# Optimization experiments

Hardware: AMD Instinct MI355X
Metric: run time of the kernel (lower is better)

The kernel has to match this reference:

```python
import jax, jax.numpy as jnp
import numpy as np

N = 8192      # total nodes = B * NPG
D = 512       # in_dim = hidden_dim = out_dim
E = 131072    # edges
B = 16        # graphs (selected_idx batch)
NPG = 512     # nodes per graph
S = 128       # selected nodes per graph
L = 3         # conv layers
EPS = 1e-5


def setup_inputs() -> dict:
    key = jax.random.key(0)
    ks = jax.random.split(key, 16)
    scale = 0.02
    return {
        "x": jax.random.normal(ks[0], (N, D), dtype=jnp.float32),
        "edge_index": jax.random.randint(ks[1], (2, E), 0, N),
        "selected_idx": jax.random.randint(ks[2], (B, S), 0, NPG),
        "edge_label": jax.random.randint(ks[3], (E,), 0, 4),
        # per-layer EdgeConv MLP params (stacked over L layers)
        "conv_W1": jax.random.normal(ks[4], (L, 2 * D, D), dtype=jnp.float32) * scale,
        "conv_b1": jnp.full((L, D), 0.01, dtype=jnp.float32),
        "conv_W2": jax.random.normal(ks[5], (L, D, D), dtype=jnp.float32) * scale,
        "conv_b2": jnp.full((L, D), 0.01, dtype=jnp.float32),
        # shared layer norms
        "ln1_g": jnp.ones((D,), dtype=jnp.float32),
        "ln1_b": jnp.zeros((D,), dtype=jnp.float32),
        "ln2_g": jnp.ones((D,), dtype=jnp.float32),
        "ln2_b": jnp.zeros((D,), dtype=jnp.float32),
        # final FFN
        "ffn_W1": jax.random.normal(ks[6], (D, D), dtype=jnp.float32) * scale,
        "ffn_b1": jnp.full((D,), 0.01, dtype=jnp.float32),
        "ffn_W2": jax.random.normal(ks[7], (D, D), dtype=jnp.float32) * scale,
        "ffn_b2": jnp.full((D,), 0.01, dtype=jnp.float32),
    }


def _layer_norm(x, g, b):
    mu = jnp.mean(x, axis=-1, keepdims=True)
    var = jnp.mean(jnp.square(x - mu), axis=-1, keepdims=True)
    return (x - mu) * jax.lax.rsqrt(var + EPS) * g + b


def reference(x, edge_index, selected_idx, edge_label,
              conv_W1, conv_b1, conv_W2, conv_b2,
              ln1_g, ln1_b, ln2_g, ln2_b,
              ffn_W1, ffn_b1, ffn_W2, ffn_b2):
    src = edge_index[0]  # x_j source nodes
    dst = edge_index[1]  # x_i target nodes (aggregation index)
    for l in range(L):
        residual = x
        h = _layer_norm(x, ln1_g, ln1_b)
        hi = h[dst]                                   # [E, D]
        hj = h[src]                                   # [E, D]
        ef = jnp.concatenate([hi, hj - hi], axis=1)   # [E, 2D]
        m = jnp.maximum(ef @ conv_W1[l] + conv_b1[l], 0.0) @ conv_W2[l] + conv_b2[l]
        agg = jax.ops.segment_max(m, dst, num_segments=N)  # max-aggregate [N, D]
        agg = jnp.where(jnp.isfinite(agg), agg, 0.0)       # nodes w/o in-edges -> 0
        x = jnp.maximum(agg, 0.0) + residual
    residual = x
    h = _layer_norm(x, ln2_g, ln2_b)
    y = jnp.maximum(h @ ffn_W1 + ffn_b1, 0.0) @ ffn_W2 + ffn_b2
    x = y + residual
    x = x.reshape(B, NPG, D)
    idx = jnp.broadcast_to(selected_idx[:, :, None], (B, S, D))
    return jnp.take_along_axis(x, idx, axis=1)  # [B, S, D]
```

## Files before the change

kernel.cpp:

```cpp
#include <hip/hip_runtime.h>
#include <stdint.h>

#define NN 8192
#define DD 512
#define EE 131072
#define BBATCH 16
#define NPG 512
#define SSEL 128
#define LL 3

typedef unsigned short u16;
typedef __bf16 bf16x8 __attribute__((ext_vector_type(8)));
typedef float f32x4 __attribute__((ext_vector_type(4)));
typedef float f32x2 __attribute__((ext_vector_type(2)));
typedef u16 u16x8 __attribute__((ext_vector_type(8)));

__device__ __forceinline__ float bf2f(u16 u) {
    union { unsigned i; float f; } v; v.i = ((unsigned)u) << 16; return v.f;
}
__device__ __forceinline__ u16 f2bf(float f) {
    union { unsigned i; float f; } v; v.f = f;
    unsigned i = v.i;
    return (u16)((i + 0x7FFFu + ((i >> 16) & 1u)) >> 16);
}

__device__ __forceinline__ unsigned pk_bf16(float s0, float s1) {
#if __has_builtin(__builtin_amdgcn_cvt_pk_bf16_f32)
    typedef __bf16 bf16x2 __attribute__((ext_vector_type(2)));
    union { bf16x2 v; unsigned u; } r;
    r.v = __builtin_amdgcn_cvt_pk_bf16_f32(s0, s1);
    return r.u;
#else
    unsigned r0 = __float_as_uint(s0);
    r0 = (r0 + 0x7FFFu + ((r0 >> 16) & 1u)) >> 16;
    unsigned r1 = __float_as_uint(s1);
    r1 = (r1 + 0x7FFFu + ((r1 >> 16) & 1u)) & 0xffff0000u;
    return r0 | r1;
#endif
}

__device__ __forceinline__ void async_cp16(const u16* g, u16* l) {
    __builtin_amdgcn_global_load_lds(
        (const __attribute__((address_space(1))) unsigned int*)g,
        (__attribute__((address_space(3))) unsigned int*)l, 16, 0, 0);
}

__global__ __launch_bounds__(256) void ln_fused(const float* __restrict__ xin,
                                                float* __restrict__ agg_io,
                                                float* __restrict__ xout,
                                                const float* __restrict__ g,
                                                const float* __restrict__ b,
                                                u16* __restrict__ h, int doAdd) {
    int row = blockIdx.x * 4 + (threadIdx.x >> 6);
    int lane = threadIdx.x & 63;
    const f32x4* x4 = (const f32x4*)(xin + (size_t)row * DD);
    f32x4 p = x4[lane * 2], q = x4[lane * 2 + 1];
    if (doAdd) {
        const f32x4* a4 = (const f32x4*)(agg_io + (size_t)row * DD);
        f32x4 pa = a4[lane * 2], qa = a4[lane * 2 + 1];
        #pragma unroll
        for (int i = 0; i < 4; ++i) { p[i] += pa[i]; q[i] += qa[i]; }
    }
    if (agg_io) {
        f32x4 z;
        #pragma unroll
        for (int i = 0; i < 4; ++i) z[i] = 0.f;
        f32x4* a4 = (f32x4*)(agg_io + (size_t)row * DD);
        a4[lane * 2] = z;
        a4[lane * 2 + 1] = z;
    }
    f32x4* xo = (f32x4*)(xout + (size_t)row * DD);
    xo[lane * 2] = p;
    xo[lane * 2 + 1] = q;
    float v[8];
    v[0] = p[0]; v[1] = p[1]; v[2] = p[2]; v[3] = p[3];
    v[4] = q[0]; v[5] = q[1]; v[6] = q[2]; v[7] = q[3];
    float s = 0.f, sq = 0.f;
    #pragma unroll
    for (int i = 0; i < 8; ++i) { s += v[i]; sq += v[i] * v[i]; }
    #pragma unroll
    for (int o = 32; o >= 1; o >>= 1) { s += __shfl_xor(s, o); sq += __shfl_xor(sq, o); }
    float mu = s * (1.f / DD);
    float var = sq * (1.f / DD) - mu * mu;
    float rs = rsqrtf(var + 1e-5f);
    int kb = lane * 8;
    u16x8 o8;
    #pragma unroll
    for (int i = 0; i < 8; ++i) o8[i] = f2bf((v[i] - mu) * rs * g[kb + i] + b[kb + i]);
    *(u16x8*)(h + (size_t)row * DD + kb) = o8;
}

__global__ void hist_kernel(const int* __restrict__ dst, int* __restrict__ cnt) {
    int e = blockIdx.x * 256 + threadIdx.x;
    if (e < EE) atomicAdd(&cnt[dst[e]], 1);
}

__global__ __launch_bounds__(1024) void scan_kernel(const int* __restrict__ cnt,
                                                    int* __restrict__ off,
                                                    int* __restrict__ cur) {
    __shared__ int part[1024];
    int t = threadIdx.x;
    int base = t * 8;
    int loc[8]; int s = 0;
    #pragma unroll
    for (int i = 0; i < 8; ++i) { loc[i] = s; s += cnt[base + i]; }
    part[t] = s;
    __syncthreads();
    for (int o = 1; o < 1024; o <<= 1) {
        int v = part[t];
        int u = (t >= o) ? part[t - o] : 0;
        __syncthreads();
        part[t] = v + u;
        __syncthreads();
    }
    int bx = (t > 0) ? part[t - 1] : 0;
    #pragma unroll
    for (int i = 0; i < 8; ++i) { off[base + i] = bx + loc[i]; cur[base + i] = bx + loc[i]; }
    if (t == 0) off[NN] = part[1023];
}

__global__ void scatter_kernel(const int* __restrict__ src, const int* __restrict__ dst,
                               int* __restrict__ cur, int* __restrict__ ssrc,
                               int* __restrict__ sdst) {
    int e = blockIdx.x * 256 + threadIdx.x;
    if (e < EE) {
        int d = dst[e];
        int p = atomicAdd(&cur[d], 1);
        ssrc[p] = src[e];
        sdst[p] = d;
    }
}

struct CvtJobs {
    const float* s[5];
    u16* d[5];
};
__global__ __launch_bounds__(256) void cvt_t5_kernel(CvtJobs jobs) {
    __shared__ u16 tile[32][33];
    const float* src = jobs.s[blockIdx.z];
    u16* dstp = jobs.d[blockIdx.z];
    int bk = blockIdx.x * 32, bn = blockIdx.y * 32;
    int tx = threadIdx.x & 31, ty = threadIdx.x >> 5;
    #pragma unroll
    for (int r = 0; r < 32; r += 8)
        tile[ty + r][tx] = f2bf(src[(size_t)(bk + ty + r) * 512 + bn + tx]);
    __syncthreads();
    #pragma unroll
    for (int r = 0; r < 32; r += 8)
        dstp[(size_t)(bn + ty + r) * 512 + bk + tx] = tile[tx][ty + r];
}

__global__ __launch_bounds__(256) void cvt_w1_kernel(const float* __restrict__ W1g,
                                                     u16* __restrict__ dstg) {
    __shared__ u16 tile[32][33];
    const float* W1 = W1g + (size_t)blockIdx.z * 1024 * 512;
    u16* dstp = dstg + (size_t)blockIdx.z * 1024 * 512;
    int bk = blockIdx.x * 32, bn = blockIdx.y * 32;
    int tx = threadIdx.x & 31, ty = threadIdx.x >> 5;
    #pragma unroll
    for (int r = 0; r < 32; r += 8) {
        int k = bk + ty + r, n = bn + tx;
        float v = (n < 512) ? (W1[(size_t)k * 512 + n] - W1[(size_t)(k + 512) * 512 + n])
                            : W1[(size_t)(k + 512) * 512 + (n - 512)];
        tile[ty + r][tx] = f2bf(v);
    }
    __syncthreads();
    #pragma unroll
    for (int r = 0; r < 32; r += 8)
        dstp[(size_t)(bn + ty + r) * 512 + bk + tx] = tile[tx][ty + r];
}

template <int EMODE>
__global__ __launch_bounds__(256) void gemm_async(
    const u16* __restrict__ A, const u16* __restrict__ BT,
    const float* __restrict__ bias, const float* __restrict__ resid,
    void* __restrict__ Cout, int K, int ldc) {
    __shared__ u16 lA[128 * 64];
    __shared__ u16 lB[128 * 64];
    const int tid = threadIdx.x;
    const int lane = tid & 63, wave = tid >> 6;
    const int wm = wave & 1, wn = wave >> 1;
    const int quad = lane >> 4, lm = lane & 15;
    const int tileM = blockIdx.x, tileN = blockIdx.y;

    const int g = (lane & 7) ^ (lane >> 3);
    const u16* ap[4];
    const u16* bp[4];
    u16* lad[4];
    u16* lbd[4];
    #pragma unroll
    for (int j = 0; j < 4; ++j) {
        int seg = wave * 4 + j;
        int rA = tileM * 128 + seg * 8 + (lane >> 3);
        int rB = tileN * 128 + seg * 8 + (lane >> 3);
        ap[j] = A + (size_t)rA * K + g * 8;
        bp[j] = BT + (size_t)rB * K + g * 8;
        lad[j] = lA + seg * 512;
        lbd[j] = lB + seg * 512;
    }

    f32x4 acc[4][4];
    #pragma unroll
    for (int mt = 0; mt < 4; ++mt)
        #pragma unroll
        for (int nt = 0; nt < 4; ++nt)
            #pragma unroll
            for (int j = 0; j < 4; ++j) acc[mt][nt][j] = 0.f;

    for (int kb = 0; kb < K; kb += 64) {
        #pragma unroll
        for (int j = 0; j < 4; ++j) {
            async_cp16(ap[j], lad[j]);
            async_cp16(bp[j], lbd[j]);
            ap[j] += 64;
            bp[j] += 64;
        }
        __syncthreads();
        #pragma unroll
        for (int kk = 0; kk < 64; kk += 32) {
            bf16x8 af[4], bfr[4];
            int gbase = (kk >> 3) + quad;
            #pragma unroll
            for (int mt = 0; mt < 4; ++mt) {
                int row = wm * 64 + mt * 16 + lm;
                af[mt] = *(const bf16x8*)(lA + row * 64 + ((gbase ^ (row & 7)) << 3));
            }
            #pragma unroll
            for (int nt = 0; nt < 4; ++nt) {
                int row = wn * 64 + nt * 16 + lm;
                bfr[nt] = *(const bf16x8*)(lB + row * 64 + ((gbase ^ (row & 7)) << 3));
            }
            #pragma unroll
            for (int mt = 0; mt < 4; ++mt)
                #pragma unroll
                for (int nt = 0; nt < 4; ++nt)
                    acc[mt][nt] = __builtin_amdgcn_mfma_f32_16x16x32_bf16(
                        af[mt], bfr[nt], acc[mt][nt], 0, 0, 0);
        }
        __syncthreads();
    }
    #pragma unroll
    for (int mt = 0; mt < 4; ++mt) {
        #pragma unroll
        for (int nt = 0; nt < 4; ++nt) {
            int col = tileN * 128 + wn * 64 + nt * 16 + lm;
            float bv;
            if (EMODE == 2) bv = 0.f;
            else if (EMODE == 3) bv = (col < 512) ? bias[col] : 0.f;
            else bv = bias[col];
            #pragma unroll
            for (int j = 0; j < 4; ++j) {
                int grow = tileM * 128 + wm * 64 + mt * 16 + quad * 4 + j;
                float v = acc[mt][nt][j] + bv;
                if (EMODE == 0) {
                    ((u16*)Cout)[(size_t)grow * ldc + col] = f2bf(fmaxf(v, 0.f));
                } else if (EMODE == 1) {
                    ((float*)Cout)[(size_t)grow * ldc + col] =
                        v + resid[(size_t)grow * ldc + col];
                } else {
                    ((u16*)Cout)[(size_t)grow * ldc + col] = f2bf(v);
                }
            }
        }
    }
}

__global__ __launch_bounds__(512, 4) void gemm_edge(
    const u16* __restrict__ P, const int* __restrict__ ssrc,
    const int* __restrict__ sdst, const u16* __restrict__ W2T,
    const float* __restrict__ b2, float* __restrict__ agg) {
    __shared__ u16 smem[128 * 64 + 256 * 64];
    __shared__ int nid_l[128];
    u16* lA = smem;
    u16* lB = smem + 128 * 64;
    const int tid = threadIdx.x;
    const int lane = tid & 63, wave = tid >> 6;
    const int wm = wave & 1, wn = wave >> 1;
    const int quad = lane >> 4, lm = lane & 15;
    const int tileN = blockIdx.x;
    const int ebase = blockIdx.y * 128;

    if (tid < 128) nid_l[tid] = sdst[ebase + tid];

    const int g = (lane & 7) ^ (lane >> 3);
    int aoff[2], boff[2];
    u16* lout[2];
    #pragma unroll
    for (int j = 0; j < 2; ++j) {
        int seg = wave * 2 + j;
        int row = seg * 8 + (lane >> 3);
        int dn = sdst[ebase + row];
        int sn = ssrc[ebase + row];
        aoff[j] = dn * 1024 + g * 8;
        boff[j] = sn * 1024 + 512 + g * 8;
        lout[j] = lA + seg * 512 + lane * 8;
    }
    int woff[4];
    u16* lbd[4];
    #pragma unroll
    for (int j = 0; j < 4; ++j) {
        int seg = wave * 4 + j;
        int row = tileN * 256 + seg * 8 + (lane >> 3);
        woff[j] = row * 512 + g * 8;
        lbd[j] = lB + seg * 512;
    }

    f32x4 acc[4][4];
    #pragma unroll
    for (int mt = 0; mt < 4; ++mt)
        #pragma unroll
        for (int nt = 0; nt < 4; ++nt)
            #pragma unroll
            for (int j = 0; j < 4; ++j) acc[mt][nt][j] = 0.f;

    for (int kb = 0; kb < 512; kb += 64) {
        u16x8 ga[2], gb[2];
        #pragma unroll
        for (int j = 0; j < 2; ++j) {
            ga[j] = *(const u16x8*)(P + aoff[j] + kb);
            gb[j] = *(const u16x8*)(P + boff[j] + kb);
        }
        #pragma unroll
        for (int j = 0; j < 4; ++j) async_cp16(W2T + woff[j] + kb, lbd[j]);
        #pragma unroll
        for (int j = 0; j < 2; ++j) {
            union { u16x8 v; unsigned w[4]; } ua, ub;
            ua.v = ga[j];
            ub.v = gb[j];
            unsigned o[4];
            #pragma unroll
            for (int q = 0; q < 4; ++q) {
                f32x2 a, c;
                a[0] = __uint_as_float(ua.w[q] << 16);
                a[1] = __uint_as_float(ua.w[q] & 0xffff0000u);
                c[0] = __uint_as_float(ub.w[q] << 16);
                c[1] = __uint_as_float(ub.w[q] & 0xffff0000u);
                f32x2 s = a + c;
#if __has_builtin(__builtin_elementwise_max)
                f32x2 z; z[0] = 0.f; z[1] = 0.f;
                s = __builtin_elementwise_max(s, z);
#else
                s[0] = fmaxf(s[0], 0.f);
                s[1] = fmaxf(s[1], 0.f);
#endif
                o[q] = pk_bf16(s[0], s[1]);
            }
            *(uint4*)lout[j] = make_uint4(o[0], o[1], o[2], o[3]);
        }
        __syncthreads();
        #pragma unroll
        for (int kk = 0; kk < 64; kk += 32) {
            bf16x8 af[4], bfr[4];
            int gbase = (kk >> 3) + quad;
            #pragma unroll
            for (int mt = 0; mt < 4; ++mt) {
                int row = wm * 64 + mt * 16 + lm;
                af[mt] = *(const bf16x8*)(lA + row * 64 + ((gbase ^ (row & 7)) << 3));
            }
            #pragma unroll
            for (int nt = 0; nt < 4; ++nt) {
                int row = wn * 64 + nt * 16 + lm;
                bfr[nt] = *(const bf16x8*)(lB + row * 64 + ((gbase ^ (row & 7)) << 3));
            }
            #pragma unroll
            for (int mt = 0; mt < 4; ++mt)
                #pragma unroll
                for (int nt = 0; nt < 4; ++nt)
                    acc[mt][nt] = __builtin_amdgcn_mfma_f32_16x16x32_bf16(
                        af[mt], bfr[nt], acc[mt][nt], 0, 0, 0);
        }
        __syncthreads();
    }

    u16* cbuf = smem;
    for (int p = 0; p < 2; ++p) {
        if (wm == p) {
            #pragma unroll
            for (int nt = 0; nt < 4; ++nt) {
                int lcol = wn * 64 + nt * 16 + lm;
                float bv = b2[tileN * 256 + lcol];
                #pragma unroll
                for (int mt = 0; mt < 4; ++mt) {
                    #pragma unroll
                    for (int j2 = 0; j2 < 4; ++j2) {
                        int row = mt * 16 + quad * 4 + j2;
                        cbuf[row * 264 + lcol] = f2bf(fmaxf(acc[mt][nt][j2] + bv, 0.f));
                    }
                }
            }
        }
        __syncthreads();
        {
            int lcol = tid & 255;
            int gcol = tileN * 256 + lcol;
            int r0 = (tid >> 8) * 32;
            int gr0 = p * 64 + r0;
            int cur = nid_l[gr0];
            float run = bf2f(cbuf[r0 * 264 + lcol]);
            for (int r = 1; r < 32; ++r) {
                int nd = nid_l[gr0 + r];
                float v = bf2f(cbuf[(r0 + r) * 264 + lcol]);
                if (nd != cur) {
                    atomicMax((unsigned int*)&agg[(size_t)cur * DD + gcol],
                              __float_as_uint(run));
                    cur = nd;
                    run = v;
                } else {
                    run = fmaxf(run, v);
                }
            }
            atomicMax((unsigned int*)&agg[(size_t)cur * DD + gcol],
                      __float_as_uint(run));
        }
        __syncthreads();
    }
}

__global__ __launch_bounds__(128) void gather_fused(const float* __restrict__ x,
                                                    const float* __restrict__ agg,
                                                    const int* __restrict__ sel,
                                                    float* __restrict__ xs) {
    int i = blockIdx.x;
    int b = i >> 7;
    int r = b * NPG + sel[i];
    const f32x4* srcp = (const f32x4*)(x + (size_t)r * DD);
    const f32x4* aggp = (const f32x4*)(agg + (size_t)r * DD);
    f32x4 v = srcp[threadIdx.x];
    f32x4 a = aggp[threadIdx.x];
    #pragma unroll
    for (int j = 0; j < 4; ++j) v[j] += a[j];
    ((f32x4*)(xs + (size_t)i * DD))[threadIdx.x] = v;
}

extern "C" void kernel_launch(void* const* d_in, const int* in_sizes, int n_in,
                              void* d_out, int out_size, void* d_ws, size_t ws_size,
                              hipStream_t stream) {
    const float* x_in = (const float*)d_in[0];
    const int* ei = (const int*)d_in[1];
    const int* sel = (const int*)d_in[2];
    const float* W1 = (const float*)d_in[4];
    const float* b1 = (const float*)d_in[5];
    const float* W2 = (const float*)d_in[6];
    const float* b2 = (const float*)d_in[7];
    const float* g1 = (const float*)d_in[8];
    const float* be1 = (const float*)d_in[9];
    const float* g2 = (const float*)d_in[10];
    const float* be2 = (const float*)d_in[11];
    const float* fW1 = (const float*)d_in[12];
    const float* fb1 = (const float*)d_in[13];
    const float* fW2 = (const float*)d_in[14];
    const float* fb2 = (const float*)d_in[15];
    float* out = (float*)d_out;

    char* w = (char*)d_ws;
    size_t off = 0;
    auto alloc = [&](size_t bytes) -> char* {
        char* p = w + off;
        off += (bytes + 255) & ~(size_t)255;
        return p;
    };
    float* xbuf = (float*)alloc((size_t)NN * DD * 4);
    float* agg  = (float*)alloc((size_t)NN * DD * 4);
    u16* h      = (u16*)alloc((size_t)NN * DD * 2);
    u16* P      = (u16*)alloc((size_t)NN * 1024 * 2);
    u16* W1T    = (u16*)alloc((size_t)LL * 1024 * DD * 2);
    u16* W2T    = (u16*)alloc((size_t)LL * DD * DD * 2);
    u16* FW1T   = (u16*)alloc((size_t)DD * DD * 2);
    u16* FW2T   = (u16*)alloc((size_t)DD * DD * 2);
    int* cnt    = (int*)alloc((size_t)NN * 4);
    int* offs   = (int*)alloc((size_t)(NN + 1) * 4);
    int* cur    = (int*)alloc((size_t)NN * 4);
    int* ssrc   = (int*)alloc((size_t)EE * 4);
    int* sdst   = (int*)alloc((size_t)EE * 4);
    float* xs   = (float*)alloc((size_t)BBATCH * SSEL * DD * 4);
    u16* hs     = (u16*)alloc((size_t)BBATCH * SSEL * DD * 2);
    u16* uu     = (u16*)alloc((size_t)BBATCH * SSEL * DD * 2);

    const int* esrc = ei;
    const int* edst = ei + EE;

    hipMemsetAsync(cnt, 0, (size_t)NN * 4, stream);
    hist_kernel<<<EE / 256, 256, 0, stream>>>(edst, cnt);
    scan_kernel<<<1, 1024, 0, stream>>>(cnt, offs, cur);
    scatter_kernel<<<EE / 256, 256, 0, stream>>>(esrc, edst, cur, ssrc, sdst);

    cvt_w1_kernel<<<dim3(16, 32, LL), 256, 0, stream>>>(W1, W1T);
    {
        CvtJobs jobs;
        jobs.s[0] = W2;
        jobs.s[1] = W2 + (size_t)DD * DD;
        jobs.s[2] = W2 + (size_t)2 * DD * DD;
        jobs.s[3] = fW1;
        jobs.s[4] = fW2;
        jobs.d[0] = W2T;
        jobs.d[1] = W2T + (size_t)DD * DD;
        jobs.d[2] = W2T + (size_t)2 * DD * DD;
        jobs.d[3] = FW1T;
        jobs.d[4] = FW2T;
        cvt_t5_kernel<<<dim3(16, 16, 5), 256, 0, stream>>>(jobs);
    }

    for (int l = 0; l < LL; ++l) {
        ln_fused<<<NN / 4, 256, 0, stream>>>(l == 0 ? x_in : xbuf, agg, xbuf, g1, be1,
                                             h, l > 0 ? 1 : 0);
        {
            dim3 grid(NN / 128, 1024 / 128);
            gemm_async<3><<<grid, 256, 0, stream>>>(
                h, W1T + (size_t)l * 1024 * DD, b1 + (size_t)l * DD, nullptr, P, DD,
                1024);
        }
        gemm_edge<<<dim3(2, EE / 128), 512, 0, stream>>>(
            P, ssrc, sdst, W2T + (size_t)l * DD * DD, b2 + (size_t)l * DD, agg);
    }

    gather_fused<<<BBATCH * SSEL, 128, 0, stream>>>(xbuf, agg, sel, xs);
    ln_fused<<<BBATCH * SSEL / 4, 256, 0, stream>>>(xs, nullptr, xs, g2, be2, hs, 0);
    dim3 gridf(BBATCH * SSEL / 128, DD / 128);
    gemm_async<0><<<gridf, 256, 0, stream>>>(hs, FW1T, fb1, nullptr, uu, DD, DD);
    gemm_async<1><<<gridf, 256, 0, stream>>>(uu, FW2T, fb2, xs, out, DD, DD);
}
```

Before: 548.4 us.

## Store source-side edge projection in fp8 and remap edge GEMM block order

```diff
diff --git a/kernel.cpp b/kernel.cpp
--- a/kernel.cpp
+++ b/kernel.cpp
@@ -10,6 +10,7 @@
 #define LL 3
 
 typedef unsigned short u16;
+typedef unsigned char u8;
 typedef __bf16 bf16x8 __attribute__((ext_vector_type(8)));
 typedef float f32x4 __attribute__((ext_vector_type(4)));
 typedef float f32x2 __attribute__((ext_vector_type(2)));
@@ -39,6 +40,39 @@
 #endif
 }
 
+__device__ __forceinline__ u8 f32_fp8(float f) {
+#if __has_builtin(__builtin_amdgcn_cvt_pk_fp8_f32)
+    return (u8)((unsigned)__builtin_amdgcn_cvt_pk_fp8_f32(f, f, 0, false) & 0xffu);
+#else
+    unsigned u = __float_as_uint(f);
+    int s = (u >> 31) & 1;
+    int exp = (int)((u >> 23) & 255) - 127;
+    unsigned man = (u >> 20) & 7;
+    if (exp < -6) return (u8)(s << 7);
+    if (exp > 8) { exp = 8; man = 7; }
+    return (u8)((s << 7) | ((exp + 7) << 3) | man);
+#endif
+}
+template <int SEL>
+__device__ __forceinline__ f32x2 fp8pair_f32(unsigned w) {
+#if __has_builtin(__builtin_amdgcn_cvt_pk_f32_fp8)
+    f32x2 r;
+    r = __builtin_amdgcn_cvt_pk_f32_fp8(w, SEL);
+    return r;
+#else
+    f32x2 r;
+    #pragma unroll
+    for (int i = 0; i < 2; ++i) {
+        unsigned u = (w >> (SEL * 16 + i * 8)) & 0xffu;
+        unsigned s = (u >> 7) & 1, e = (u >> 3) & 15, m = u & 7;
+        float v = (e == 0) ? (float)m * 0.001953125f
+                           : (float)(8 + m) * exp2f((float)e - 10.f);
+        r[i] = s ? -v : v;
+    }
+    return r;
+#endif
+}
+
 __device__ __forceinline__ void async_cp16(const u16* g, u16* l) {
     __builtin_amdgcn_global_load_lds(
         (const __attribute__((address_space(1))) unsigned int*)g,
@@ -174,7 +208,7 @@
 __global__ __launch_bounds__(256) void gemm_async(
     const u16* __restrict__ A, const u16* __restrict__ BT,
     const float* __restrict__ bias, const float* __restrict__ resid,
-    void* __restrict__ Cout, int K, int ldc) {
+    void* __restrict__ Cout, u8* __restrict__ CoutB, int K, int ldc) {
     __shared__ u16 lA[128 * 64];
     __shared__ u16 lB[128 * 64];
     const int tid = threadIdx.x;
@@ -257,6 +291,11 @@
                 } else if (EMODE == 1) {
                     ((float*)Cout)[(size_t)grow * ldc + col] =
                         v + resid[(size_t)grow * ldc + col];
+                } else if (EMODE == 3) {
+                    if (col < 512)
+                        ((u16*)Cout)[(size_t)grow * 512 + col] = f2bf(v);
+                    else
+                        CoutB[(size_t)grow * 512 + (col - 512)] = f32_fp8(v);
                 } else {
                     ((u16*)Cout)[(size_t)grow * ldc + col] = f2bf(v);
                 }
@@ -266,19 +305,21 @@
 }
 
 __global__ __launch_bounds__(512, 4) void gemm_edge(
-    const u16* __restrict__ P, const int* __restrict__ ssrc,
-    const int* __restrict__ sdst, const u16* __restrict__ W2T,
-    const float* __restrict__ b2, float* __restrict__ agg) {
+    const u16* __restrict__ Pa, const u8* __restrict__ Pb8,
+    const int* __restrict__ ssrc, const int* __restrict__ sdst,
+    const u16* __restrict__ W2T, const float* __restrict__ b2,
+    float* __restrict__ agg) {
     __shared__ u16 smem[128 * 64 + 256 * 64];
     __shared__ int nid_l[128];
     u16* lA = smem;
     u16* lB = smem + 128 * 64;
+    const int bid = blockIdx.x;
+    const int tileN = (bid >> 3) & 1;
+    const int ebase = ((((bid >> 4) << 3) | (bid & 7))) * 128;
     const int tid = threadIdx.x;
     const int lane = tid & 63, wave = tid >> 6;
     const int wm = wave & 1, wn = wave >> 1;
     const int quad = lane >> 4, lm = lane & 15;
-    const int tileN = blockIdx.x;
-    const int ebase = blockIdx.y * 128;
 
     if (tid < 128) nid_l[tid] = sdst[ebase + tid];
 
@@ -291,8 +332,8 @@
         int row = seg * 8 + (lane >> 3);
         int dn = sdst[ebase + row];
         int sn = ssrc[ebase + row];
-        aoff[j] = dn * 1024 + g * 8;
-        boff[j] = sn * 1024 + 512 + g * 8;
+        aoff[j] = dn * 512 + g * 8;
+        boff[j] = sn * 512 + g * 8;
         lout[j] = lA + seg * 512 + lane * 8;
     }
     int woff[4];
@@ -314,35 +355,34 @@
             for (int j = 0; j < 4; ++j) acc[mt][nt][j] = 0.f;
 
     for (int kb = 0; kb < 512; kb += 64) {
-        u16x8 ga[2], gb[2];
+        u16x8 ga[2];
+        uint2 gb[2];
         #pragma unroll
         for (int j = 0; j < 2; ++j) {
-            ga[j] = *(const u16x8*)(P + aoff[j] + kb);
-            gb[j] = *(const u16x8*)(P + boff[j] + kb);
+            ga[j] = *(const u16x8*)(Pa + aoff[j] + kb);
+            gb[j] = *(const uint2*)(Pb8 + boff[j] + kb);
         }
         #pragma unroll
         for (int j = 0; j < 4; ++j) async_cp16(W2T + woff[j] + kb, lbd[j]);
         #pragma unroll
         for (int j = 0; j < 2; ++j) {
-            union { u16x8 v; unsigned w[4]; } ua, ub;
+            union { u16x8 v; unsigned w[4]; } ua;
             ua.v = ga[j];
-            ub.v = gb[j];
+            unsigned pw0 = gb[j].x, pw1 = gb[j].y;
+            f32x2 c0 = fp8pair_f32<0>(pw0);
+            f32x2 c1 = fp8pair_f32<1>(pw0);
+            f32x2 c2 = fp8pair_f32<0>(pw1);
+            f32x2 c3 = fp8pair_f32<1>(pw1);
             unsigned o[4];
             #pragma unroll
             for (int q = 0; q < 4; ++q) {
                 f32x2 a, c;
                 a[0] = __uint_as_float(ua.w[q] << 16);
                 a[1] = __uint_as_float(ua.w[q] & 0xffff0000u);
-                c[0] = __uint_as_float(ub.w[q] << 16);
-                c[1] = __uint_as_float(ub.w[q] & 0xffff0000u);
+                c = (q == 0) ? c0 : (q == 1) ? c1 : (q == 2) ? c2 : c3;
                 f32x2 s = a + c;
-#if __has_builtin(__builtin_elementwise_max)
-                f32x2 z; z[0] = 0.f; z[1] = 0.f;
-                s = __builtin_elementwise_max(s, z);
-#else
                 s[0] = fmaxf(s[0], 0.f);
                 s[1] = fmaxf(s[1], 0.f);
-#endif
                 o[q] = pk_bf16(s[0], s[1]);
             }
             *(uint4*)lout[j] = make_uint4(o[0], o[1], o[2], o[3]);
@@ -462,7 +502,8 @@
     float* xbuf = (float*)alloc((size_t)NN * DD * 4);
     float* agg  = (float*)alloc((size_t)NN * DD * 4);
     u16* h      = (u16*)alloc((size_t)NN * DD * 2);
-    u16* P      = (u16*)alloc((size_t)NN * 1024 * 2);
+    u16* Pa     = (u16*)alloc((size_t)NN * DD * 2);
+    u8* Pb8     = (u8*)alloc((size_t)NN * DD);
     u16* W1T    = (u16*)alloc((size_t)LL * 1024 * DD * 2);
     u16* W2T    = (u16*)alloc((size_t)LL * DD * DD * 2);
     u16* FW1T   = (u16*)alloc((size_t)DD * DD * 2);
@@ -479,7 +520,7 @@
     const int* esrc = ei;
     const int* edst = ei + EE;
 
-    hipMemsetAsync(cnt, 0, (size_t)NN * 4, stream);
+    (void)hipMemsetAsync(cnt, 0, (size_t)NN * 4, stream);
     hist_kernel<<<EE / 256, 256, 0, stream>>>(edst, cnt);
     scan_kernel<<<1, 1024, 0, stream>>>(cnt, offs, cur);
     scatter_kernel<<<EE / 256, 256, 0, stream>>>(esrc, edst, cur, ssrc, sdst);
@@ -506,16 +547,17 @@
         {
             dim3 grid(NN / 128, 1024 / 128);
             gemm_async<3><<<grid, 256, 0, stream>>>(
-                h, W1T + (size_t)l * 1024 * DD, b1 + (size_t)l * DD, nullptr, P, DD,
-                1024);
-        }
-        gemm_edge<<<dim3(2, EE / 128), 512, 0, stream>>>(
-            P, ssrc, sdst, W2T + (size_t)l * DD * DD, b2 + (size_t)l * DD, agg);
+                h, W1T + (size_t)l * 1024 * DD, b1 + (size_t)l * DD, nullptr, Pa, Pb8,
+                DD, 512);
+        }
+        gemm_edge<<<2 * (EE / 128), 512, 0, stream>>>(
+            Pa, Pb8, ssrc, sdst, W2T + (size_t)l * DD * DD, b2 + (size_t)l * DD, agg);
     }
 
     gather_fused<<<BBATCH * SSEL, 128, 0, stream>>>(xbuf, agg, sel, xs);
     ln_fused<<<BBATCH * SSEL / 4, 256, 0, stream>>>(xs, nullptr, xs, g2, be2, hs, 0);
     dim3 gridf(BBATCH * SSEL / 128, DD / 128);
-    gemm_async<0><<<gridf, 256, 0, stream>>>(hs, FW1T, fb1, nullptr, uu, DD, DD);
-    gemm_async<1><<<gridf, 256, 0, stream>>>(uu, FW2T, fb2, xs, out, DD, DD);
-}
+    gemm_async<0><<<gridf, 256, 0, stream>>>(hs, FW1T, fb1, nullptr, uu, nullptr, DD,
+                                             DD);
+    gemm_async<1><<<gridf, 256, 0, stream>>>(uu, FW2T, fb2, xs, out, nullptr, DD, DD);
+}
```

New measurement: 588.7 us. +7.4%, slower.

## Switch edge GEMM second layer to FP8 MFMA with scaled FP8 weights

Applied to the files above, without the earlier changes.

```diff
diff --git a/kernel.cpp b/kernel.cpp
--- a/kernel.cpp
+++ b/kernel.cpp
@@ -8,8 +8,10 @@
 #define NPG 512
 #define SSEL 128
 #define LL 3
+#define LSTR 36
 
 typedef unsigned short u16;
+typedef unsigned char u8;
 typedef __bf16 bf16x8 __attribute__((ext_vector_type(8)));
 typedef float f32x4 __attribute__((ext_vector_type(4)));
 typedef float f32x2 __attribute__((ext_vector_type(2)));
@@ -24,18 +26,29 @@
     return (u16)((i + 0x7FFFu + ((i >> 16) & 1u)) >> 16);
 }
 
-__device__ __forceinline__ unsigned pk_bf16(float s0, float s1) {
-#if __has_builtin(__builtin_amdgcn_cvt_pk_bf16_f32)
-    typedef __bf16 bf16x2 __attribute__((ext_vector_type(2)));
-    union { bf16x2 v; unsigned u; } r;
-    r.v = __builtin_amdgcn_cvt_pk_bf16_f32(s0, s1);
-    return r.u;
+__device__ __forceinline__ u8 f32_fp8_sw(float f) {
+    unsigned u = __float_as_uint(f);
+    int s = (u >> 31) & 1;
+    int exp = (int)((u >> 23) & 255) - 127;
+    unsigned man = (u >> 20) & 7;
+    if (exp < -6) return (u8)(s << 7);
+    if (exp > 8) { exp = 8; man = 7; }
+    return (u8)((s << 7) | ((exp + 7) << 3) | man);
+}
+__device__ __forceinline__ u8 f32_fp8(float f) {
+#if __has_builtin(__builtin_amdgcn_cvt_pk_fp8_f32)
+    return (u8)((unsigned)__builtin_amdgcn_cvt_pk_fp8_f32(f, f, 0, false) & 0xffu);
 #else
-    unsigned r0 = __float_as_uint(s0);
-    r0 = (r0 + 0x7FFFu + ((r0 >> 16) & 1u)) >> 16;
-    unsigned r1 = __float_as_uint(s1);
-    r1 = (r1 + 0x7FFFu + ((r1 >> 16) & 1u)) & 0xffff0000u;
-    return r0 | r1;
+    return f32_fp8_sw(f);
+#endif
+}
+template <bool HI>
+__device__ __forceinline__ unsigned pk2_fp8(float s0, float s1, unsigned old) {
+#if __has_builtin(__builtin_amdgcn_cvt_pk_fp8_f32)
+    return (unsigned)__builtin_amdgcn_cvt_pk_fp8_f32(s0, s1, (int)old, HI);
+#else
+    unsigned pair = (unsigned)f32_fp8_sw(s0) | ((unsigned)f32_fp8_sw(s1) << 8);
+    return HI ? ((old & 0xffffu) | (pair << 16)) : ((old & 0xffff0000u) | pair);
 #endif
 }
 
@@ -132,10 +145,10 @@
 }
 
 struct CvtJobs {
-    const float* s[5];
-    u16* d[5];
+    const float* s[2];
+    u16* d[2];
 };
-__global__ __launch_bounds__(256) void cvt_t5_kernel(CvtJobs jobs) {
+__global__ __launch_bounds__(256) void cvt_t2_kernel(CvtJobs jobs) {
     __shared__ u16 tile[32][33];
     const float* src = jobs.s[blockIdx.z];
     u16* dstp = jobs.d[blockIdx.z];
@@ -148,6 +161,22 @@
     #pragma unroll
     for (int r = 0; r < 32; r += 8)
         dstp[(size_t)(bn + ty + r) * 512 + bk + tx] = tile[tx][ty + r];
+}
+
+__global__ __launch_bounds__(256) void cvt_w28_kernel(const float* __restrict__ W2g,
+                                                      u8* __restrict__ dstg) {
+    __shared__ float tile[32][33];
+    const float* W2 = W2g + (size_t)blockIdx.z * 512 * 512;
+    u8* dstp = dstg + (size_t)blockIdx.z * 512 * 512;
+    int bk = blockIdx.x * 32, bn = blockIdx.y * 32;
+    int tx = threadIdx.x & 31, ty = threadIdx.x >> 5;
+    #pragma unroll
+    for (int r = 0; r < 32; r += 8)
+        tile[ty + r][tx] = W2[(size_t)(bk + ty + r) * 512 + bn + tx] * 16.f;
+    __syncthreads();
+    #pragma unroll
+    for (int r = 0; r < 32; r += 8)
+        dstp[(size_t)(bn + ty + r) * 512 + bk + tx] = f32_fp8(tile[tx][ty + r]);
 }
 
 __global__ __launch_bounds__(256) void cvt_w1_kernel(const float* __restrict__ W1g,
@@ -245,8 +274,7 @@
         for (int nt = 0; nt < 4; ++nt) {
             int col = tileN * 128 + wn * 64 + nt * 16 + lm;
             float bv;
-            if (EMODE == 2) bv = 0.f;
-            else if (EMODE == 3) bv = (col < 512) ? bias[col] : 0.f;
+            if (EMODE == 3) bv = (col < 512) ? bias[col] : 0.f;
             else bv = bias[col];
             #pragma unroll
             for (int j = 0; j < 4; ++j) {
@@ -267,12 +295,12 @@
 
 __global__ __launch_bounds__(512, 4) void gemm_edge(
     const u16* __restrict__ P, const int* __restrict__ ssrc,
-    const int* __restrict__ sdst, const u16* __restrict__ W2T,
+    const int* __restrict__ sdst, const u8* __restrict__ W28T,
     const float* __restrict__ b2, float* __restrict__ agg) {
-    __shared__ u16 smem[128 * 64 + 256 * 64];
+    __shared__ u16 smem[16896];
     __shared__ int nid_l[128];
     u16* lA = smem;
-    u16* lB = smem + 128 * 64;
+    u16* lB = smem + 128 * LSTR;
     const int tid = threadIdx.x;
     const int lane = tid & 63, wave = tid >> 6;
     const int wm = wave & 1, wn = wave >> 1;
@@ -282,7 +310,7 @@
 
     if (tid < 128) nid_l[tid] = sdst[ebase + tid];
 
-    const int g = (lane & 7) ^ (lane >> 3);
+    const int g = lane & 7;
     int aoff[2], boff[2];
     u16* lout[2];
     #pragma unroll
@@ -293,17 +321,10 @@
         int sn = ssrc[ebase + row];
         aoff[j] = dn * 1024 + g * 8;
         boff[j] = sn * 1024 + 512 + g * 8;
-        lout[j] = lA + seg * 512 + lane * 8;
-    }
-    int woff[4];
-    u16* lbd[4];
-    #pragma unroll
-    for (int j = 0; j < 4; ++j) {
-        int seg = wave * 4 + j;
-        int row = tileN * 256 + seg * 8 + (lane >> 3);
-        woff[j] = row * 512 + g * 8;
-        lbd[j] = lB + seg * 512;
-    }
+        lout[j] = lA + row * LSTR + g * 4;
+    }
+    const int brow = tid >> 3;
+    const int bg = tid & 7;
 
     f32x4 acc[4][4];
     #pragma unroll
@@ -314,20 +335,25 @@
             for (int j = 0; j < 4; ++j) acc[mt][nt][j] = 0.f;
 
     for (int kb = 0; kb < 512; kb += 64) {
+        uint2 bw[4];
+        #pragma unroll
+        for (int j = 0; j < 4; ++j) {
+            int lrow = j * 64 + brow;
+            bw[j] = *(const uint2*)(W28T + (size_t)(tileN * 256 + lrow) * 512 + kb +
+                                    bg * 8);
+        }
         u16x8 ga[2], gb[2];
         #pragma unroll
         for (int j = 0; j < 2; ++j) {
             ga[j] = *(const u16x8*)(P + aoff[j] + kb);
             gb[j] = *(const u16x8*)(P + boff[j] + kb);
         }
-        #pragma unroll
-        for (int j = 0; j < 4; ++j) async_cp16(W2T + woff[j] + kb, lbd[j]);
         #pragma unroll
         for (int j = 0; j < 2; ++j) {
             union { u16x8 v; unsigned w[4]; } ua, ub;
             ua.v = ga[j];
             ub.v = gb[j];
-            unsigned o[4];
+            f32x2 s[4];
             #pragma unroll
             for (int q = 0; q < 4; ++q) {
                 f32x2 a, c;
@@ -335,39 +361,41 @@
                 a[1] = __uint_as_float(ua.w[q] & 0xffff0000u);
                 c[0] = __uint_as_float(ub.w[q] << 16);
                 c[1] = __uint_as_float(ub.w[q] & 0xffff0000u);
-                f32x2 s = a + c;
-#if __has_builtin(__builtin_elementwise_max)
-                f32x2 z; z[0] = 0.f; z[1] = 0.f;
-                s = __builtin_elementwise_max(s, z);
-#else
-                s[0] = fmaxf(s[0], 0.f);
-                s[1] = fmaxf(s[1], 0.f);
-#endif
-                o[q] = pk_bf16(s[0], s[1]);
-            }
-            *(uint4*)lout[j] = make_uint4(o[0], o[1], o[2], o[3]);
-        }
+                f32x2 t = a + c;
+                t[0] = fmaxf(t[0], 0.f);
+                t[1] = fmaxf(t[1], 0.f);
+                s[q] = t;
+            }
+            unsigned d0 = pk2_fp8<false>(s[0][0], s[0][1], 0u);
+            d0 = pk2_fp8<true>(s[1][0], s[1][1], d0);
+            unsigned d1 = pk2_fp8<false>(s[2][0], s[2][1], 0u);
+            d1 = pk2_fp8<true>(s[3][0], s[3][1], d1);
+            *(uint2*)lout[j] = make_uint2(d0, d1);
+        }
+        #pragma unroll
+        for (int j = 0; j < 4; ++j)
+            *(uint2*)(lB + (j * 64 + brow) * LSTR + bg * 4) = bw[j];
         __syncthreads();
         #pragma unroll
         for (int kk = 0; kk < 64; kk += 32) {
-            bf16x8 af[4], bfr[4];
-            int gbase = (kk >> 3) + quad;
+            long af[4], bf[4];
+            int gq = (kk >> 3) + quad;
             #pragma unroll
             for (int mt = 0; mt < 4; ++mt) {
                 int row = wm * 64 + mt * 16 + lm;
-                af[mt] = *(const bf16x8*)(lA + row * 64 + ((gbase ^ (row & 7)) << 3));
+                af[mt] = *(const long*)(lA + row * LSTR + gq * 4);
             }
             #pragma unroll
             for (int nt = 0; nt < 4; ++nt) {
                 int row = wn * 64 + nt * 16 + lm;
-                bfr[nt] = *(const bf16x8*)(lB + row * 64 + ((gbase ^ (row & 7)) << 3));
+                bf[nt] = *(const long*)(lB + row * LSTR + gq * 4);
             }
             #pragma unroll
             for (int mt = 0; mt < 4; ++mt)
                 #pragma unroll
                 for (int nt = 0; nt < 4; ++nt)
-                    acc[mt][nt] = __builtin_amdgcn_mfma_f32_16x16x32_bf16(
-                        af[mt], bfr[nt], acc[mt][nt], 0, 0, 0);
+                    acc[mt][nt] = __builtin_amdgcn_mfma_f32_16x16x32_fp8_fp8(
+                        af[mt], bf[nt], acc[mt][nt], 0, 0, 0);
         }
         __syncthreads();
     }
@@ -384,7 +412,8 @@
                     #pragma unroll
                     for (int j2 = 0; j2 < 4; ++j2) {
                         int row = mt * 16 + quad * 4 + j2;
-                        cbuf[row * 264 + lcol] = f2bf(fmaxf(acc[mt][nt][j2] + bv, 0.f));
+                        cbuf[row * 264 + lcol] =
+                            f2bf(fmaxf(acc[mt][nt][j2] * 0.0625f + bv, 0.f));
                     }
                 }
             }
@@ -464,7 +493,7 @@
     u16* h      = (u16*)alloc((size_t)NN * DD * 2);
     u16* P      = (u16*)alloc((size_t)NN * 1024 * 2);
     u16* W1T    = (u16*)alloc((size_t)LL * 1024 * DD * 2);
-    u16* W2T    = (u16*)alloc((size_t)LL * DD * DD * 2);
+    u8* W28T    = (u8*)alloc((size_t)LL * DD * DD);
     u16* FW1T   = (u16*)alloc((size_t)DD * DD * 2);
     u16* FW2T   = (u16*)alloc((size_t)DD * DD * 2);
     int* cnt    = (int*)alloc((size_t)NN * 4);
@@ -479,25 +508,20 @@
     const int* esrc = ei;
     const int* edst = ei + EE;
 
-    hipMemsetAsync(cnt, 0, (size_t)NN * 4, stream);
+    (void)hipMemsetAsync(cnt, 0, (size_t)NN * 4, stream);
     hist_kernel<<<EE / 256, 256, 0, stream>>>(edst, cnt);
     scan_kernel<<<1, 1024, 0, stream>>>(cnt, offs, cur);
     scatter_kernel<<<EE / 256, 256, 0, stream>>>(esrc, edst, cur, ssrc, sdst);
 
     cvt_w1_kernel<<<dim3(16, 32, LL), 256, 0, stream>>>(W1, W1T);
+    cvt_w28_kernel<<<dim3(16, 16, LL), 256, 0, stream>>>(W2, W28T);
     {
         CvtJobs jobs;
-        jobs.s[0] = W2;
-        jobs.s[1] = W2 + (size_t)DD * DD;
-        jobs.s[2] = W2 + (size_t)2 * DD * DD;
-        jobs.s[3] = fW1;
-        jobs.s[4] = fW2;
-        jobs.d[0] = W2T;
-        jobs.d[1] = W2T + (size_t)DD * DD;
-        jobs.d[2] = W2T + (size_t)2 * DD * DD;
-        jobs.d[3] = FW1T;
-        jobs.d[4] = FW2T;
-        cvt_t5_kernel<<<dim3(16, 16, 5), 256, 0, stream>>>(jobs);
+        jobs.s[0] = fW1;
+        jobs.s[1] = fW2;
+        jobs.d[0] = FW1T;
+        jobs.d[1] = FW2T;
+        cvt_t2_kernel<<<dim3(16, 16, 2), 256, 0, stream>>>(jobs);
     }
 
     for (int l = 0; l < LL; ++l) {
@@ -510,7 +534,7 @@
                 1024);
         }
         gemm_edge<<<dim3(2, EE / 128), 512, 0, stream>>>(
-            P, ssrc, sdst, W2T + (size_t)l * DD * DD, b2 + (size_t)l * DD, agg);
+            P, ssrc, sdst, W28T + (size_t)l * DD * DD, b2 + (size_t)l * DD, agg);
     }
 
     gather_fused<<<BBATCH * SSEL, 128, 0, stream>>>(xbuf, agg, sel, xs);
```

Measured after the change: 585.0 us. +6.7%, slower.
